# Performance work log

Hardware: AMD Instinct MI355X
Metric: run time of the kernel (lower is better)

The kernel has to match this reference:

```python
import jax, jax.numpy as jnp
import numpy as np

H, KV, DH = 16, 4, 64  # num_heads, num_kv_heads, head_dim


def setup_inputs() -> dict:
    key = jax.random.key(0)
    k1, k2, k3, k4, k5 = jax.random.split(key, 5)
    B, L, D = 1, 4096, 1024
    s = 0.02
    return {
        "x": jax.random.normal(k1, (B, L, D), dtype=jnp.float32),
        "Wq": jax.random.normal(k2, (D, H * DH), dtype=jnp.float32) * s,
        "Wk": jax.random.normal(k3, (D, KV * DH), dtype=jnp.float32) * s,
        "Wv": jax.random.normal(k4, (D, KV * DH), dtype=jnp.float32) * s,
        "Wo": jax.random.normal(k5, (H * DH, D), dtype=jnp.float32) * s,
    }


def _rotate_half(t):
    t1, t2 = t[..., : DH // 2], t[..., DH // 2 :]
    return jnp.concatenate([-t2, t1], axis=-1)


def reference(x, Wq, Wk, Wv, Wo):
    B, L, D = x.shape
    G = H // KV  # query heads per kv head
    q = (x @ Wq).reshape(B, L, H, DH)
    k = (x @ Wk).reshape(B, L, KV, DH)
    v = (x @ Wv).reshape(B, L, KV, DH)

    # RoPE: inv_freq over even dims, angles duplicated across both halves
    inv_freq = 1.0 / (10000.0 ** (jnp.arange(0, DH, 2, dtype=jnp.float32) / DH))
    t = jnp.arange(L, dtype=jnp.float32)
    freqs = t[:, None] * inv_freq[None, :]                 # [L, DH/2]
    emb = jnp.concatenate([freqs, freqs], axis=-1)[None, :, None, :]  # [1,L,1,DH]
    cos, sin = jnp.cos(emb), jnp.sin(emb)
    q = q * cos + _rotate_half(q) * sin
    k = k * cos + _rotate_half(k) * sin

    # GQA: query head h attends with kv head h // G (repeat_interleave layout)
    qg = q.reshape(B, L, KV, G, DH)
    scale = DH ** -0.5
    attn = jnp.einsum("bqkgd,bskd->bkgqs", qg, k) * scale  # [B,KV,G,L,L]
    attn = jax.nn.softmax(attn, axis=-1)
    out = jnp.einsum("bkgqs,bskd->bqkgd", attn, v).reshape(B, L, H * DH)
    return out @ Wo
```

## Files before the change

### kernel.cpp

```cpp
#include <hip/hip_runtime.h>
#include <math.h>

#define L 4096
#define D 1024
#define H 16
#define KV 4
#define DH 64

typedef __attribute__((ext_vector_type(8))) short bf16x8;
typedef __attribute__((ext_vector_type(4))) float f32x4;
typedef __attribute__((ext_vector_type(16))) float f32x16;
typedef __attribute__((ext_vector_type(2))) unsigned int u32x2;

static __device__ __forceinline__ unsigned short f2bf(float f) {
    unsigned u = __float_as_uint(f);
    u = (u + 0x7FFF + ((u >> 16) & 1)) >> 16;
    return (unsigned short)u;
}

static __device__ __forceinline__ bf16x8 mk8(unsigned a, unsigned b, unsigned c, unsigned d) {
    union { unsigned u[4]; bf16x8 v; } x;
    x.u[0] = a; x.u[1] = b; x.u[2] = c; x.u[3] = d;
    return x.v;
}

#define EXP2F(x) __builtin_amdgcn_exp2f(x)
#define ZERO16 ((f32x16){0.f,0.f,0.f,0.f,0.f,0.f,0.f,0.f,0.f,0.f,0.f,0.f,0.f,0.f,0.f,0.f})

#define GLD16(src, dst) \
    __builtin_amdgcn_global_load_lds((__attribute__((address_space(1))) void*)(src), \
                                     (__attribute__((address_space(3))) void*)(dst), 16, 0, 0)

__global__ __launch_bounds__(256) void prep_kernel(
        const float* __restrict__ x,  const float* __restrict__ Wq,
        const float* __restrict__ Wk, const float* __restrict__ Wv,
        const float* __restrict__ Wo,
        unsigned short* __restrict__ xb, unsigned short* __restrict__ WqkvT,
        unsigned short* __restrict__ WoT) {
    const int b = blockIdx.x, tid = threadIdx.x;
    if (b < 4096) {
        int i = (b * 256 + tid) * 4;
        float4 v = *(const float4*)&x[i];
        ushort4 o;
        o.x = f2bf(v.x); o.y = f2bf(v.y); o.z = f2bf(v.z); o.w = f2bf(v.w);
        *(ushort4*)&xb[i] = o;
        return;
    }
    __shared__ float t[32][33];
    const float* src; unsigned short* dst; int N, n0, k0;
    if (b < 5120)      { int tq = b - 4096; src = Wq; dst = WqkvT;                     N = 1024; n0 = (tq & 31) * 32; k0 = (tq >> 5) * 32; }
    else if (b < 5376) { int tq = b - 5120; src = Wk; dst = WqkvT + (size_t)1024*1024; N = 256;  n0 = (tq & 7)  * 32; k0 = (tq >> 3) * 32; }
    else if (b < 5632) { int tq = b - 5376; src = Wv; dst = WqkvT + (size_t)1280*1024; N = 256;  n0 = (tq & 7)  * 32; k0 = (tq >> 3) * 32; }
    else               { int tq = b - 5632; src = Wo; dst = WoT;                       N = 1024; n0 = (tq & 31) * 32; k0 = (tq >> 5) * 32; }
    const int tx = tid & 31, ty = tid >> 5;
    #pragma unroll
    for (int j = 0; j < 4; ++j)
        t[ty + 8 * j][tx] = src[(size_t)(k0 + ty + 8 * j) * N + n0 + tx];
    __syncthreads();
    #pragma unroll
    for (int j = 0; j < 4; ++j)
        dst[(size_t)(n0 + ty + 8 * j) * 1024 + k0 + tx] = f2bf(t[tx][ty + 8 * j]);
}

__global__ __launch_bounds__(256) void gemm_bf16(const unsigned short* __restrict__ A,
                                                 const unsigned short* __restrict__ BT,
                                                 float* __restrict__ C,
                                                 int M, int N, int K) {
    __shared__ unsigned short As[128 * 32];
    __shared__ unsigned short Bs[128 * 32];

    const int tid  = threadIdx.x;
    const int w    = tid >> 6;
    const int lane = tid & 63;
    const int c    = lane & 15;
    const int quad = lane >> 4;
    const int wy = w >> 1, wx = w & 1;
    const int row0 = blockIdx.y * 128;
    const int col0 = blockIdx.x * 128;

    const int ld_row = w * 16 + (lane >> 2);
    const int ld_col = (lane & 3) * 8;

    f32x4 acc[4][4];
    #pragma unroll
    for (int mt = 0; mt < 4; ++mt)
        #pragma unroll
        for (int nt = 0; nt < 4; ++nt)
            acc[mt][nt] = (f32x4){0.f, 0.f, 0.f, 0.f};

    for (int k0 = 0; k0 < K; k0 += 32) {
        __syncthreads();
        GLD16(&A [(size_t)(row0 + ld_row)      * K + k0 + ld_col], &As[w * 512]);
        GLD16(&A [(size_t)(row0 + ld_row + 64) * K + k0 + ld_col], &As[w * 512 + 2048]);
        GLD16(&BT[(size_t)(col0 + ld_row)      * K + k0 + ld_col], &Bs[w * 512]);
        GLD16(&BT[(size_t)(col0 + ld_row + 64) * K + k0 + ld_col], &Bs[w * 512 + 2048]);
        __syncthreads();

        bf16x8 af[4], bfr[4];
        #pragma unroll
        for (int mt = 0; mt < 4; ++mt)
            af[mt] = *(const bf16x8*)&As[(wy * 64 + mt * 16 + c) * 32 + quad * 8];
        #pragma unroll
        for (int nt = 0; nt < 4; ++nt)
            bfr[nt] = *(const bf16x8*)&Bs[(wx * 64 + nt * 16 + c) * 32 + quad * 8];

        #pragma unroll
        for (int mt = 0; mt < 4; ++mt)
            #pragma unroll
            for (int nt = 0; nt < 4; ++nt)
                acc[mt][nt] = __builtin_amdgcn_mfma_f32_16x16x32_bf16(af[mt], bfr[nt], acc[mt][nt], 0, 0, 0);
    }

    #pragma unroll
    for (int mt = 0; mt < 4; ++mt)
        #pragma unroll
        for (int nt = 0; nt < 4; ++nt)
            #pragma unroll
            for (int r = 0; r < 4; ++r)
                C[(size_t)(row0 + wy * 64 + mt * 16 + quad * 4 + r) * N
                  + col0 + wx * 64 + nt * 16 + c] = acc[mt][nt][r];
}

__global__ __launch_bounds__(256) void gemm_qkv_rope(
        const unsigned short* __restrict__ A,
        const unsigned short* __restrict__ BT,
        unsigned short* __restrict__ qb,
        unsigned short* __restrict__ kbuf,
        unsigned short* __restrict__ vbT) {
    __shared__ unsigned short As[128 * 32];
    __shared__ unsigned short Bs[128 * 32];

    const int tid  = threadIdx.x;
    const int w    = tid >> 6;
    const int lane = tid & 63;
    const int c    = lane & 15;
    const int quad = lane >> 4;
    const int wy = w >> 1, wx = w & 1;
    const int row0 = blockIdx.y * 128;
    const int col0 = blockIdx.x * 128;

    const int ld_row = w * 16 + (lane >> 2);
    const int ld_col = (lane & 3) * 8;

    f32x4 acc[4][4];
    #pragma unroll
    for (int mt = 0; mt < 4; ++mt)
        #pragma unroll
        for (int nt = 0; nt < 4; ++nt)
            acc[mt][nt] = (f32x4){0.f, 0.f, 0.f, 0.f};

    for (int k0 = 0; k0 < 1024; k0 += 32) {
        __syncthreads();
        GLD16(&A [(size_t)(row0 + ld_row)      * 1024 + k0 + ld_col], &As[w * 512]);
        GLD16(&A [(size_t)(row0 + ld_row + 64) * 1024 + k0 + ld_col], &As[w * 512 + 2048]);
        GLD16(&BT[(size_t)(col0 + ld_row)      * 1024 + k0 + ld_col], &Bs[w * 512]);
        GLD16(&BT[(size_t)(col0 + ld_row + 64) * 1024 + k0 + ld_col], &Bs[w * 512 + 2048]);
        __syncthreads();

        bf16x8 af[4], bfr[4];
        #pragma unroll
        for (int mt = 0; mt < 4; ++mt)
            af[mt] = *(const bf16x8*)&As[(wy * 64 + mt * 16 + c) * 32 + quad * 8];
        #pragma unroll
        for (int nt = 0; nt < 4; ++nt)
            bfr[nt] = *(const bf16x8*)&Bs[(wx * 64 + nt * 16 + c) * 32 + quad * 8];

        #pragma unroll
        for (int mt = 0; mt < 4; ++mt)
            #pragma unroll
            for (int nt = 0; nt < 4; ++nt)
                acc[mt][nt] = __builtin_amdgcn_mfma_f32_16x16x32_bf16(af[mt], bfr[nt], acc[mt][nt], 0, 0, 0);
    }

    const int colb = col0 + wx * 64;
    if (colb < 1280) {
        unsigned short* dst; int hh, hstride; float scale;
        if (colb < 1024) { dst = qb;   hh = colb >> 6;          hstride = H;  scale = 0.18033688011112042f; }
        else             { dst = kbuf; hh = (colb - 1024) >> 6; hstride = KV; scale = 1.0f; }
        #pragma unroll
        for (int nt = 0; nt < 2; ++nt) {
            int d = nt * 16 + c;
            float invf = EXP2F((float)d * -0.4152410118609203f);
            #pragma unroll
            for (int mt = 0; mt < 4; ++mt)
                #pragma unroll
                for (int r = 0; r < 4; ++r) {
                    int l = row0 + wy * 64 + mt * 16 + quad * 4 + r;
                    float ang = (float)l * invf;
                    float sn = __sinf(ang), cs = __cosf(ang);
                    float x1 = acc[mt][nt][r], x2 = acc[mt][nt + 2][r];
                    dst[((size_t)l * hstride + hh) * DH + d]      = f2bf((x1 * cs - x2 * sn) * scale);
                    dst[((size_t)l * hstride + hh) * DH + d + 32] = f2bf((x2 * cs + x1 * sn) * scale);
                }
        }
    } else {
        int vh = (colb - 1280) >> 6;
        #pragma unroll
        for (int nt = 0; nt < 4; ++nt)
            #pragma unroll
            for (int mt = 0; mt < 4; ++mt) {
                int l = row0 + wy * 64 + mt * 16 + quad * 4;
                ushort4 o;
                o.x = f2bf(acc[mt][nt][0]); o.y = f2bf(acc[mt][nt][1]);
                o.z = f2bf(acc[mt][nt][2]); o.w = f2bf(acc[mt][nt][3]);
                *(ushort4*)&vbT[(size_t)(vh * DH + nt * 16 + c) * L + l] = o;
            }
    }
}

__global__ __attribute__((amdgpu_flat_work_group_size(512, 512), amdgpu_waves_per_eu(2)))
void attn_mfma_kernel(
        const unsigned short* __restrict__ qb,
        const unsigned short* __restrict__ kb,
        const unsigned short* __restrict__ vbT,
        unsigned short* __restrict__ ob) {
    __shared__ __align__(16) float Ep[4][64][64];
    __shared__ __align__(16) float Rs[8][2][32];

    const int tid  = threadIdx.x;
    const int w    = tid >> 6;
    const int lane = tid & 63;
    const int c32  = lane & 31;
    const int hi   = lane >> 5;
    const int g    = w >> 2;
    const int kv = blockIdx.y;
    const int h  = kv * 4 + (w & 3);
    const int q0 = blockIdx.x * 64;
    const int s_base = g * 2048;

    bf16x8 qf[2][4];
    {
        const unsigned short* qbase = qb + ((size_t)(q0 + c32) * H + h) * DH + hi * 8;
        #pragma unroll
        for (int qt = 0; qt < 2; ++qt)
            #pragma unroll
            for (int kd = 0; kd < 4; ++kd)
                qf[qt][kd] = *(const bf16x8*)&qbase[qt * 32 * H * DH + kd * 16];
    }

    f32x16 oacc[2][2];
    #pragma unroll
    for (int qt = 0; qt < 2; ++qt)
        #pragma unroll
        for (int dt = 0; dt < 2; ++dt)
            oacc[qt][dt] = ZERO16;
    float rsum[2] = {0.f, 0.f};

    const unsigned short* kbase  = kb  + ((size_t)(s_base + c32) * KV + kv) * DH + hi * 8;
    const unsigned short* vTbase = vbT + (size_t)(kv * DH) * L + s_base + hi * 8;

    bf16x8 kf[2][4];
    #pragma unroll
    for (int a = 0; a < 2; ++a)
        #pragma unroll
        for (int kd = 0; kd < 4; ++kd)
            kf[a][kd] = *(const bf16x8*)&kbase[a * 32 * KV * DH + kd * 16];

    for (int it = 0; it < 32; ++it) {
        bf16x8 vfrag[2][4];
        #pragma unroll
        for (int dt = 0; dt < 2; ++dt)
            #pragma unroll
            for (int ck = 0; ck < 4; ++ck)
                vfrag[dt][ck] = *(const bf16x8*)&vTbase[(size_t)(dt * 32 + c32) * L
                                                        + it * 64 + ck * 16];

        const int itn = (it + 1) & 31;

        #pragma unroll
        for (int kt2 = 0; kt2 < 2; ++kt2) {
            bf16x8 pf[2][2];
            #pragma unroll
            for (int qt = 0; qt < 2; ++qt) {
                f32x16 s = ZERO16;
                #pragma unroll
                for (int kd = 0; kd < 4; ++kd)
                    s = __builtin_amdgcn_mfma_f32_32x32x16_bf16(kf[kt2][kd], qf[qt][kd], s, 0, 0, 0);
                float p[16];
                #pragma unroll
                for (int r = 0; r < 16; ++r)
                    p[r] = __uint_as_float(__float_as_uint(EXP2F(s[r])) & 0xFFFF0000u);
                float t0 = (p[0] + p[1]) + (p[2] + p[3]);
                float t1 = (p[4] + p[5]) + (p[6] + p[7]);
                float t2 = (p[8] + p[9]) + (p[10] + p[11]);
                float t3 = (p[12] + p[13]) + (p[14] + p[15]);
                rsum[qt] += (t0 + t1) + (t2 + t3);
                unsigned u[8];
                #pragma unroll
                for (int i = 0; i < 8; ++i)
                    u[i] = __builtin_amdgcn_perm(__float_as_uint(p[2 * i + 1]),
                                                 __float_as_uint(p[2 * i]), 0x07060302u);
                #pragma unroll
                for (int f = 0; f < 2; ++f) {
                    u32x2 e0 = __builtin_amdgcn_permlane32_swap(u[4 * f + 0], u[4 * f + 2], false, false);
                    u32x2 e1 = __builtin_amdgcn_permlane32_swap(u[4 * f + 1], u[4 * f + 3], false, false);
                    pf[qt][f] = mk8(e0.x, e1.x, e0.y, e1.y);
                }
            }
            if (kt2 == 1) {
                #pragma unroll
                for (int a = 0; a < 2; ++a)
                    #pragma unroll
                    for (int kd = 0; kd < 4; ++kd)
                        kf[a][kd] = *(const bf16x8*)&kbase[((size_t)itn * 64 + a * 32) * KV * DH + kd * 16];
            }
            __builtin_amdgcn_s_setprio(1);
            #pragma unroll
            for (int dt = 0; dt < 2; ++dt)
                #pragma unroll
                for (int f = 0; f < 2; ++f) {
                    bf16x8 vf = vfrag[dt][kt2 * 2 + f];
                    #pragma unroll
                    for (int qt = 0; qt < 2; ++qt)
                        oacc[qt][dt] = __builtin_amdgcn_mfma_f32_32x32x16_bf16(pf[qt][f], vf, oacc[qt][dt], 0, 0, 0);
                }
            __builtin_amdgcn_s_setprio(0);
        }
    }

    #pragma unroll
    for (int qt = 0; qt < 2; ++qt) {
        u32x2 e = __builtin_amdgcn_permlane32_swap(__float_as_uint(rsum[qt]),
                                                   __float_as_uint(rsum[qt]), false, false);
        float tot = __uint_as_float(e.x) + __uint_as_float(e.y);
        Rs[w][qt][c32] = tot;
    }
    if (g == 1) {
        #pragma unroll
        for (int qt = 0; qt < 2; ++qt)
            #pragma unroll
            for (int dt = 0; dt < 2; ++dt) {
                const int d = dt * 32 + c32;
                #pragma unroll
                for (int rr = 0; rr < 4; ++rr) {
                    const int gq = (qt * 8 + 2 * rr + hi) ^ (d & 15);
                    f32x4 val = {oacc[qt][dt][rr * 4 + 0], oacc[qt][dt][rr * 4 + 1],
                                 oacc[qt][dt][rr * 4 + 2], oacc[qt][dt][rr * 4 + 3]};
                    *(f32x4*)&Ep[w - 4][d][gq * 4] = val;
                }
            }
    }
    __syncthreads();
    if (g == 0) {
        #pragma unroll
        for (int qt = 0; qt < 2; ++qt)
            #pragma unroll
            for (int dt = 0; dt < 2; ++dt) {
                const int d = dt * 32 + c32;
                #pragma unroll
                for (int rr = 0; rr < 4; ++rr) {
                    const int gq = (qt * 8 + 2 * rr + hi) ^ (d & 15);
                    f32x4 val = *(const f32x4*)&Ep[w][d][gq * 4];
                    oacc[qt][dt][rr * 4 + 0] += val[0];
                    oacc[qt][dt][rr * 4 + 1] += val[1];
                    oacc[qt][dt][rr * 4 + 2] += val[2];
                    oacc[qt][dt][rr * 4 + 3] += val[3];
                }
            }
        #pragma unroll
        for (int qt = 0; qt < 2; ++qt)
            #pragma unroll
            for (int rr = 0; rr < 4; ++rr) {
                f32x4 ra = *(const f32x4*)&Rs[w][qt][8 * rr + 4 * hi];
                f32x4 rb = *(const f32x4*)&Rs[w + 4][qt][8 * rr + 4 * hi];
                #pragma unroll
                for (int i = 0; i < 4; ++i) {
                    float inv = 1.0f / (ra[i] + rb[i]);
                    int row = q0 + qt * 32 + 8 * rr + 4 * hi + i;
                    #pragma unroll
                    for (int dt = 0; dt < 2; ++dt)
                        ob[(size_t)row * (H * DH) + h * DH + dt * 32 + c32] =
                            f2bf(oacc[qt][dt][rr * 4 + i] * inv);
                }
            }
    }
}

extern "C" void kernel_launch(void* const* d_in, const int* in_sizes, int n_in,
                              void* d_out, int out_size, void* d_ws, size_t ws_size,
                              hipStream_t stream) {
    const float* x  = (const float*)d_in[0];
    const float* Wq = (const float*)d_in[1];
    const float* Wk = (const float*)d_in[2];
    const float* Wv = (const float*)d_in[3];
    const float* Wo = (const float*)d_in[4];
    float* out = (float*)d_out;

    char* ws = (char*)d_ws;
    unsigned short* xb    = (unsigned short*)ws;
    unsigned short* ob    = xb;
    unsigned short* qb    = (unsigned short*)(ws + 8388608);
    unsigned short* kb    = (unsigned short*)(ws + 16777216);
    unsigned short* vbT   = (unsigned short*)(ws + 18874368);
    unsigned short* WqkvT = (unsigned short*)(ws + 20971520);
    unsigned short* WoT   = (unsigned short*)(ws + 24117248);

    dim3 blk(256);

    prep_kernel<<<6656, blk, 0, stream>>>(x, Wq, Wk, Wv, Wo, xb, WqkvT, WoT);

    gemm_qkv_rope<<<dim3(12, 32), blk, 0, stream>>>(xb, WqkvT, qb, kb, vbT);

    attn_mfma_kernel<<<dim3(L / 64, KV), dim3(512), 0, stream>>>(qb, kb, vbT, ob);

    gemm_bf16<<<dim3(D / 128, L / 128), blk, 0, stream>>>(ob, WoT, out, L, D, D);
}
```

Measured before the change: 256.1 us.

## Halve attention query tile, stage V via LDS double buffer, raise occupancy

The attention kernel now handles 32 queries per block instead of 64, which halves the accumulator and Q registers and doubles the grid. V tiles are loaded asynchronously into a double-buffered, XOR-swizzled LDS buffer shared by the four heads of a KV group, instead of each wave loading them from global memory. The waves-per-EU hint goes from 2 to 4. Together these aim for higher occupancy and less redundant V traffic, at the cost of a barrier per iteration and K reloads amortised over fewer queries.

```diff
diff --git a/kernel.cpp b/kernel.cpp
--- a/kernel.cpp
+++ b/kernel.cpp
@@ -208,14 +208,14 @@
     }
 }
 
-__global__ __attribute__((amdgpu_flat_work_group_size(512, 512), amdgpu_waves_per_eu(2)))
+__global__ __attribute__((amdgpu_flat_work_group_size(512, 512), amdgpu_waves_per_eu(4)))
 void attn_mfma_kernel(
         const unsigned short* __restrict__ qb,
         const unsigned short* __restrict__ kb,
         const unsigned short* __restrict__ vbT,
         unsigned short* __restrict__ ob) {
-    __shared__ __align__(16) float Ep[4][64][64];
-    __shared__ __align__(16) float Rs[8][2][32];
+    __shared__ __align__(16) unsigned short Vt[2][2][64][64];
+    __shared__ __align__(16) float Rs[8][32];
 
     const int tid  = threadIdx.x;
     const int w    = tid >> 6;
@@ -225,29 +225,29 @@
     const int g    = w >> 2;
     const int kv = blockIdx.y;
     const int h  = kv * 4 + (w & 3);
-    const int q0 = blockIdx.x * 64;
+    const int q0 = blockIdx.x * 32;
     const int s_base = g * 2048;
 
-    bf16x8 qf[2][4];
+    const int vrow0 = (w & 3) * 16;
+    const int d0 = vrow0 + (lane >> 3);
+    const unsigned short* vsrc0 = vbT + (size_t)(kv * DH + d0) * L + s_base
+                                  + (((lane & 7) ^ (d0 & 7)) << 3);
+    const unsigned short* vsrc1 = vbT + (size_t)(kv * DH + d0 + 8) * L + s_base
+                                  + (((lane & 7) ^ ((d0 + 8) & 7)) << 3);
+
+    bf16x8 qf[4];
     {
         const unsigned short* qbase = qb + ((size_t)(q0 + c32) * H + h) * DH + hi * 8;
         #pragma unroll
-        for (int qt = 0; qt < 2; ++qt)
-            #pragma unroll
-            for (int kd = 0; kd < 4; ++kd)
-                qf[qt][kd] = *(const bf16x8*)&qbase[qt * 32 * H * DH + kd * 16];
-    }
-
-    f32x16 oacc[2][2];
-    #pragma unroll
-    for (int qt = 0; qt < 2; ++qt)
-        #pragma unroll
-        for (int dt = 0; dt < 2; ++dt)
-            oacc[qt][dt] = ZERO16;
-    float rsum[2] = {0.f, 0.f};
-
-    const unsigned short* kbase  = kb  + ((size_t)(s_base + c32) * KV + kv) * DH + hi * 8;
-    const unsigned short* vTbase = vbT + (size_t)(kv * DH) * L + s_base + hi * 8;
+        for (int kd = 0; kd < 4; ++kd)
+            qf[kd] = *(const bf16x8*)&qbase[kd * 16];
+    }
+
+    f32x16 oacc[2];
+    oacc[0] = ZERO16; oacc[1] = ZERO16;
+    float rsum = 0.f;
+
+    const unsigned short* kbase = kb + ((size_t)(s_base + c32) * KV + kv) * DH + hi * 8;
 
     bf16x8 kf[2][4];
     #pragma unroll
@@ -255,47 +255,47 @@
         #pragma unroll
         for (int kd = 0; kd < 4; ++kd)
             kf[a][kd] = *(const bf16x8*)&kbase[a * 32 * KV * DH + kd * 16];
+    GLD16(vsrc0, &Vt[g][0][vrow0][0]);
+    GLD16(vsrc1, &Vt[g][0][vrow0 + 8][0]);
 
     for (int it = 0; it < 32; ++it) {
-        bf16x8 vfrag[2][4];
-        #pragma unroll
-        for (int dt = 0; dt < 2; ++dt)
-            #pragma unroll
-            for (int ck = 0; ck < 4; ++ck)
-                vfrag[dt][ck] = *(const bf16x8*)&vTbase[(size_t)(dt * 32 + c32) * L
-                                                        + it * 64 + ck * 16];
-
+        const int buf = it & 1;
+        __syncthreads();
+
+        if (it != 31) {
+            GLD16(vsrc0 + (it + 1) * 64, &Vt[g][buf ^ 1][vrow0][0]);
+            GLD16(vsrc1 + (it + 1) * 64, &Vt[g][buf ^ 1][vrow0 + 8][0]);
+        }
         const int itn = (it + 1) & 31;
 
         #pragma unroll
         for (int kt2 = 0; kt2 < 2; ++kt2) {
-            bf16x8 pf[2][2];
-            #pragma unroll
-            for (int qt = 0; qt < 2; ++qt) {
-                f32x16 s = ZERO16;
-                #pragma unroll
-                for (int kd = 0; kd < 4; ++kd)
-                    s = __builtin_amdgcn_mfma_f32_32x32x16_bf16(kf[kt2][kd], qf[qt][kd], s, 0, 0, 0);
-                float p[16];
-                #pragma unroll
-                for (int r = 0; r < 16; ++r)
-                    p[r] = __uint_as_float(__float_as_uint(EXP2F(s[r])) & 0xFFFF0000u);
-                float t0 = (p[0] + p[1]) + (p[2] + p[3]);
-                float t1 = (p[4] + p[5]) + (p[6] + p[7]);
-                float t2 = (p[8] + p[9]) + (p[10] + p[11]);
-                float t3 = (p[12] + p[13]) + (p[14] + p[15]);
-                rsum[qt] += (t0 + t1) + (t2 + t3);
-                unsigned u[8];
-                #pragma unroll
-                for (int i = 0; i < 8; ++i)
-                    u[i] = __builtin_amdgcn_perm(__float_as_uint(p[2 * i + 1]),
-                                                 __float_as_uint(p[2 * i]), 0x07060302u);
-                #pragma unroll
-                for (int f = 0; f < 2; ++f) {
-                    u32x2 e0 = __builtin_amdgcn_permlane32_swap(u[4 * f + 0], u[4 * f + 2], false, false);
-                    u32x2 e1 = __builtin_amdgcn_permlane32_swap(u[4 * f + 1], u[4 * f + 3], false, false);
-                    pf[qt][f] = mk8(e0.x, e1.x, e0.y, e1.y);
-                }
+            f32x16 s = ZERO16;
+            #pragma unroll
+            for (int kd = 0; kd < 4; ++kd)
+                s = __builtin_amdgcn_mfma_f32_32x32x16_bf16(kf[kt2][kd], qf[kd], s, 0, 0, 0);
+
+            unsigned u[8];
+            #pragma unroll
+            for (int hf = 0; hf < 2; ++hf) {
+                float ph[8];
+                #pragma unroll
+                for (int r = 0; r < 8; ++r)
+                    ph[r] = __uint_as_float(__float_as_uint(EXP2F(s[hf * 8 + r])) & 0xFFFF0000u);
+                float t0 = (ph[0] + ph[1]) + (ph[2] + ph[3]);
+                float t1 = (ph[4] + ph[5]) + (ph[6] + ph[7]);
+                rsum += t0 + t1;
+                #pragma unroll
+                for (int i = 0; i < 4; ++i)
+                    u[hf * 4 + i] = __builtin_amdgcn_perm(__float_as_uint(ph[2 * i + 1]),
+                                                          __float_as_uint(ph[2 * i]), 0x07060302u);
+            }
+            bf16x8 pf[2];
+            #pragma unroll
+            for (int f = 0; f < 2; ++f) {
+                u32x2 e0 = __builtin_amdgcn_permlane32_swap(u[4 * f + 0], u[4 * f + 2], false, false);
+                u32x2 e1 = __builtin_amdgcn_permlane32_swap(u[4 * f + 1], u[4 * f + 3], false, false);
+                pf[f] = mk8(e0.x, e1.x, e0.y, e1.y);
             }
             if (kt2 == 1) {
                 #pragma unroll
@@ -309,70 +309,65 @@
             for (int dt = 0; dt < 2; ++dt)
                 #pragma unroll
                 for (int f = 0; f < 2; ++f) {
-                    bf16x8 vf = vfrag[dt][kt2 * 2 + f];
-                    #pragma unroll
-                    for (int qt = 0; qt < 2; ++qt)
-                        oacc[qt][dt] = __builtin_amdgcn_mfma_f32_32x32x16_bf16(pf[qt][f], vf, oacc[qt][dt], 0, 0, 0);
+                    bf16x8 vf = *(const bf16x8*)&Vt[g][buf][dt * 32 + c32]
+                                    [(((kt2 * 4 + f * 2 + hi) ^ (c32 & 7)) << 3)];
+                    oacc[dt] = __builtin_amdgcn_mfma_f32_32x32x16_bf16(pf[f], vf, oacc[dt], 0, 0, 0);
                 }
             __builtin_amdgcn_s_setprio(0);
         }
     }
 
-    #pragma unroll
-    for (int qt = 0; qt < 2; ++qt) {
-        u32x2 e = __builtin_amdgcn_permlane32_swap(__float_as_uint(rsum[qt]),
-                                                   __float_as_uint(rsum[qt]), false, false);
-        float tot = __uint_as_float(e.x) + __uint_as_float(e.y);
-        Rs[w][qt][c32] = tot;
-    }
+    float tot;
+    {
+        u32x2 e = __builtin_amdgcn_permlane32_swap(__float_as_uint(rsum),
+                                                   __float_as_uint(rsum), false, false);
+        tot = __uint_as_float(e.x) + __uint_as_float(e.y);
+    }
+    __syncthreads();
+    float (*Ep)[64][32] = (float (*)[64][32])(&Vt[0][0][0][0]);
+    Rs[w][c32] = tot;
     if (g == 1) {
         #pragma unroll
-        for (int qt = 0; qt < 2; ++qt)
-            #pragma unroll
-            for (int dt = 0; dt < 2; ++dt) {
-                const int d = dt * 32 + c32;
-                #pragma unroll
-                for (int rr = 0; rr < 4; ++rr) {
-                    const int gq = (qt * 8 + 2 * rr + hi) ^ (d & 15);
-                    f32x4 val = {oacc[qt][dt][rr * 4 + 0], oacc[qt][dt][rr * 4 + 1],
-                                 oacc[qt][dt][rr * 4 + 2], oacc[qt][dt][rr * 4 + 3]};
-                    *(f32x4*)&Ep[w - 4][d][gq * 4] = val;
-                }
-            }
+        for (int dt = 0; dt < 2; ++dt) {
+            const int d = dt * 32 + c32;
+            #pragma unroll
+            for (int rr = 0; rr < 4; ++rr) {
+                const int gq = (2 * rr + hi) ^ (d & 7);
+                f32x4 val = {oacc[dt][rr * 4 + 0], oacc[dt][rr * 4 + 1],
+                             oacc[dt][rr * 4 + 2], oacc[dt][rr * 4 + 3]};
+                *(f32x4*)&Ep[w - 4][d][gq * 4] = val;
+            }
+        }
     }
     __syncthreads();
     if (g == 0) {
         #pragma unroll
-        for (int qt = 0; qt < 2; ++qt)
-            #pragma unroll
-            for (int dt = 0; dt < 2; ++dt) {
-                const int d = dt * 32 + c32;
-                #pragma unroll
-                for (int rr = 0; rr < 4; ++rr) {
-                    const int gq = (qt * 8 + 2 * rr + hi) ^ (d & 15);
-                    f32x4 val = *(const f32x4*)&Ep[w][d][gq * 4];
-                    oacc[qt][dt][rr * 4 + 0] += val[0];
-                    oacc[qt][dt][rr * 4 + 1] += val[1];
-                    oacc[qt][dt][rr * 4 + 2] += val[2];
-                    oacc[qt][dt][rr * 4 + 3] += val[3];
-                }
-            }
-        #pragma unroll
-        for (int qt = 0; qt < 2; ++qt)
+        for (int dt = 0; dt < 2; ++dt) {
+            const int d = dt * 32 + c32;
             #pragma unroll
             for (int rr = 0; rr < 4; ++rr) {
-                f32x4 ra = *(const f32x4*)&Rs[w][qt][8 * rr + 4 * hi];
-                f32x4 rb = *(const f32x4*)&Rs[w + 4][qt][8 * rr + 4 * hi];
-                #pragma unroll
-                for (int i = 0; i < 4; ++i) {
-                    float inv = 1.0f / (ra[i] + rb[i]);
-                    int row = q0 + qt * 32 + 8 * rr + 4 * hi + i;
-                    #pragma unroll
-                    for (int dt = 0; dt < 2; ++dt)
-                        ob[(size_t)row * (H * DH) + h * DH + dt * 32 + c32] =
-                            f2bf(oacc[qt][dt][rr * 4 + i] * inv);
-                }
-            }
+                const int gq = (2 * rr + hi) ^ (d & 7);
+                f32x4 val = *(const f32x4*)&Ep[w][d][gq * 4];
+                oacc[dt][rr * 4 + 0] += val[0];
+                oacc[dt][rr * 4 + 1] += val[1];
+                oacc[dt][rr * 4 + 2] += val[2];
+                oacc[dt][rr * 4 + 3] += val[3];
+            }
+        }
+        #pragma unroll
+        for (int rr = 0; rr < 4; ++rr) {
+            f32x4 ra = *(const f32x4*)&Rs[w][8 * rr + 4 * hi];
+            f32x4 rb = *(const f32x4*)&Rs[w + 4][8 * rr + 4 * hi];
+            #pragma unroll
+            for (int i = 0; i < 4; ++i) {
+                float inv = 1.0f / (ra[i] + rb[i]);
+                int row = q0 + 8 * rr + 4 * hi + i;
+                #pragma unroll
+                for (int dt = 0; dt < 2; ++dt)
+                    ob[(size_t)row * (H * DH) + h * DH + dt * 32 + c32] =
+                        f2bf(oacc[dt][rr * 4 + i] * inv);
+            }
+        }
     }
 }
 
@@ -401,7 +396,7 @@
 
     gemm_qkv_rope<<<dim3(12, 32), blk, 0, stream>>>(xb, WqkvT, qb, kb, vbT);
 
-    attn_mfma_kernel<<<dim3(L / 64, KV), dim3(512), 0, stream>>>(qb, kb, vbT, ob);
+    attn_mfma_kernel<<<dim3(L / 32, KV), dim3(512), 0, stream>>>(qb, kb, vbT, ob);
 
     gemm_bf16<<<dim3(D / 128, L / 128), blk, 0, stream>>>(ob, WoT, out, L, D, D);
 }
```

Result: slower. 279.1 us (+9.0%).

## Stage V tiles in double-buffered swizzled LDS shared across head waves

Applied to the files above, without the earlier changes.

Each group of four waves (one per query head sharing a KV head) previously loaded identical V fragments from global memory on its own. Now V tiles of 128 keys are loaded once per group with direct global-to-LDS loads (GLD16) into a double-buffered, XOR-swizzled LDS buffer. Waves then read their fragments from LDS. The K register tile is doubled to 128 keys per iteration, and the epilogue LDS buffer is aliased onto the V staging area. This cuts redundant global/L2 traffic but adds a block-wide barrier every iteration and more register pressure from the larger K tile.

```diff
diff --git a/kernel.cpp b/kernel.cpp
--- a/kernel.cpp
+++ b/kernel.cpp
@@ -214,7 +214,7 @@
         const unsigned short* __restrict__ kb,
         const unsigned short* __restrict__ vbT,
         unsigned short* __restrict__ ob) {
-    __shared__ __align__(16) float Ep[4][64][64];
+    __shared__ __align__(16) unsigned short Vt[2][2][64][128];
     __shared__ __align__(16) float Rs[8][2][32];
 
     const int tid  = threadIdx.x;
@@ -228,6 +228,16 @@
     const int q0 = blockIdx.x * 64;
     const int s_base = g * 2048;
 
+    const int vrow0 = (w & 3) * 16;
+    const unsigned short* vsrc[4];
+    #pragma unroll
+    for (int s = 0; s < 4; ++s) {
+        int d = vrow0 + s * 4 + (lane >> 4);
+        int swz = (d & 15) ^ (((d >> 4) & 1) << 2);
+        vsrc[s] = vbT + (size_t)(kv * DH + d) * L + s_base + (((lane & 15) ^ swz) << 3);
+    }
+    const int swzr = (c32 & 15) ^ ((c32 >> 4) << 2);
+
     bf16x8 qf[2][4];
     {
         const unsigned short* qbase = qb + ((size_t)(q0 + c32) * H + h) * DH + hi * 8;
@@ -246,29 +256,31 @@
             oacc[qt][dt] = ZERO16;
     float rsum[2] = {0.f, 0.f};
 
-    const unsigned short* kbase  = kb  + ((size_t)(s_base + c32) * KV + kv) * DH + hi * 8;
-    const unsigned short* vTbase = vbT + (size_t)(kv * DH) * L + s_base + hi * 8;
-
-    bf16x8 kf[2][4];
-    #pragma unroll
-    for (int a = 0; a < 2; ++a)
+    const unsigned short* kbase = kb + ((size_t)(s_base + c32) * KV + kv) * DH + hi * 8;
+
+    bf16x8 kf[4][4];
+    #pragma unroll
+    for (int a = 0; a < 4; ++a)
         #pragma unroll
         for (int kd = 0; kd < 4; ++kd)
             kf[a][kd] = *(const bf16x8*)&kbase[a * 32 * KV * DH + kd * 16];
-
-    for (int it = 0; it < 32; ++it) {
-        bf16x8 vfrag[2][4];
-        #pragma unroll
-        for (int dt = 0; dt < 2; ++dt)
-            #pragma unroll
-            for (int ck = 0; ck < 4; ++ck)
-                vfrag[dt][ck] = *(const bf16x8*)&vTbase[(size_t)(dt * 32 + c32) * L
-                                                        + it * 64 + ck * 16];
-
-        const int itn = (it + 1) & 31;
-
-        #pragma unroll
-        for (int kt2 = 0; kt2 < 2; ++kt2) {
+    #pragma unroll
+    for (int s = 0; s < 4; ++s)
+        GLD16(vsrc[s], &Vt[g][0][vrow0 + s * 4][0]);
+
+    for (int it = 0; it < 16; ++it) {
+        const int buf = it & 1;
+        __syncthreads();
+
+        if (it != 15) {
+            #pragma unroll
+            for (int s = 0; s < 4; ++s)
+                GLD16(vsrc[s] + (size_t)(it + 1) * 128, &Vt[g][buf ^ 1][vrow0 + s * 4][0]);
+        }
+        const int itn = (it + 1) & 15;
+
+        #pragma unroll
+        for (int kt2 = 0; kt2 < 4; ++kt2) {
             bf16x8 pf[2][2];
             #pragma unroll
             for (int qt = 0; qt < 2; ++qt) {
@@ -297,19 +309,20 @@
                     pf[qt][f] = mk8(e0.x, e1.x, e0.y, e1.y);
                 }
             }
-            if (kt2 == 1) {
-                #pragma unroll
-                for (int a = 0; a < 2; ++a)
+            if (kt2 == 3) {
+                #pragma unroll
+                for (int a = 0; a < 4; ++a)
                     #pragma unroll
                     for (int kd = 0; kd < 4; ++kd)
-                        kf[a][kd] = *(const bf16x8*)&kbase[((size_t)itn * 64 + a * 32) * KV * DH + kd * 16];
+                        kf[a][kd] = *(const bf16x8*)&kbase[((size_t)itn * 128 + a * 32) * KV * DH + kd * 16];
             }
             __builtin_amdgcn_s_setprio(1);
             #pragma unroll
             for (int dt = 0; dt < 2; ++dt)
                 #pragma unroll
                 for (int f = 0; f < 2; ++f) {
-                    bf16x8 vf = vfrag[dt][kt2 * 2 + f];
+                    bf16x8 vf = *(const bf16x8*)&Vt[g][buf][dt * 32 + c32]
+                                    [((kt2 * 4 + f * 2 + hi) ^ swzr) << 3];
                     #pragma unroll
                     for (int qt = 0; qt < 2; ++qt)
                         oacc[qt][dt] = __builtin_amdgcn_mfma_f32_32x32x16_bf16(pf[qt][f], vf, oacc[qt][dt], 0, 0, 0);
@@ -325,6 +338,8 @@
         float tot = __uint_as_float(e.x) + __uint_as_float(e.y);
         Rs[w][qt][c32] = tot;
     }
+    __syncthreads();
+    float (*Ep)[64][64] = (float (*)[64][64])&Vt[0][0][0][0];
     if (g == 1) {
         #pragma unroll
         for (int qt = 0; qt < 2; ++qt)
```

New measurement: 381.1 us. 1.49x slower.

## Split attention key range four ways and stage V tiles through LDS

Applied to the files above, without the earlier changes.

The attention block grows from 512 to 1024 threads, so the key dimension is split across four wave groups of 1024 keys each instead of two groups of 2048. V is now loaded into swizzled, double-buffered LDS tiles with async global-to-LDS copies (GLD16) rather than per-lane strided global reads. The end-of-kernel reduction combines four partial accumulators and row sums through LDS. The aim is more waves per CU for latency hiding and coalesced V traffic, at the cost of a barrier every iteration and a longer, multi-barrier reduction.

```diff
diff --git a/kernel.cpp b/kernel.cpp
--- a/kernel.cpp
+++ b/kernel.cpp
@@ -208,14 +208,14 @@
     }
 }
 
-__global__ __attribute__((amdgpu_flat_work_group_size(512, 512), amdgpu_waves_per_eu(2)))
+__global__ __attribute__((amdgpu_flat_work_group_size(1024, 1024), amdgpu_waves_per_eu(4)))
 void attn_mfma_kernel(
         const unsigned short* __restrict__ qb,
         const unsigned short* __restrict__ kb,
         const unsigned short* __restrict__ vbT,
         unsigned short* __restrict__ ob) {
-    __shared__ __align__(16) float Ep[4][64][64];
-    __shared__ __align__(16) float Rs[8][2][32];
+    __shared__ __align__(16) unsigned short Vt[4][2][64][64];
+    __shared__ __align__(16) float Rs[16][2][32];
 
     const int tid  = threadIdx.x;
     const int w    = tid >> 6;
@@ -226,7 +226,14 @@
     const int kv = blockIdx.y;
     const int h  = kv * 4 + (w & 3);
     const int q0 = blockIdx.x * 64;
-    const int s_base = g * 2048;
+    const int s_base = g * 1024;
+
+    const int vrow0 = (w & 3) * 16;
+    const int d0 = vrow0 + (lane >> 3);
+    const unsigned short* vsrc0 = vbT + (size_t)(kv * DH + d0) * L + s_base
+                                  + (((lane & 7) ^ (d0 & 7)) << 3);
+    const unsigned short* vsrc1 = vbT + (size_t)(kv * DH + d0 + 8) * L + s_base
+                                  + (((lane & 7) ^ ((d0 + 8) & 7)) << 3);
 
     bf16x8 qf[2][4];
     {
@@ -246,8 +253,7 @@
             oacc[qt][dt] = ZERO16;
     float rsum[2] = {0.f, 0.f};
 
-    const unsigned short* kbase  = kb  + ((size_t)(s_base + c32) * KV + kv) * DH + hi * 8;
-    const unsigned short* vTbase = vbT + (size_t)(kv * DH) * L + s_base + hi * 8;
+    const unsigned short* kbase = kb + ((size_t)(s_base + c32) * KV + kv) * DH + hi * 8;
 
     bf16x8 kf[2][4];
     #pragma unroll
@@ -255,17 +261,18 @@
         #pragma unroll
         for (int kd = 0; kd < 4; ++kd)
             kf[a][kd] = *(const bf16x8*)&kbase[a * 32 * KV * DH + kd * 16];
-
-    for (int it = 0; it < 32; ++it) {
-        bf16x8 vfrag[2][4];
-        #pragma unroll
-        for (int dt = 0; dt < 2; ++dt)
-            #pragma unroll
-            for (int ck = 0; ck < 4; ++ck)
-                vfrag[dt][ck] = *(const bf16x8*)&vTbase[(size_t)(dt * 32 + c32) * L
-                                                        + it * 64 + ck * 16];
-
-        const int itn = (it + 1) & 31;
+    GLD16(vsrc0, &Vt[g][0][vrow0][0]);
+    GLD16(vsrc1, &Vt[g][0][vrow0 + 8][0]);
+
+    for (int it = 0; it < 16; ++it) {
+        const int buf = it & 1;
+        __syncthreads();
+
+        if (it != 15) {
+            GLD16(vsrc0 + (it + 1) * 64, &Vt[g][buf ^ 1][vrow0][0]);
+            GLD16(vsrc1 + (it + 1) * 64, &Vt[g][buf ^ 1][vrow0 + 8][0]);
+        }
+        const int itn = (it + 1) & 15;
 
         #pragma unroll
         for (int kt2 = 0; kt2 < 2; ++kt2) {
@@ -309,7 +316,8 @@
             for (int dt = 0; dt < 2; ++dt)
                 #pragma unroll
                 for (int f = 0; f < 2; ++f) {
-                    bf16x8 vf = vfrag[dt][kt2 * 2 + f];
+                    bf16x8 vf = *(const bf16x8*)&Vt[g][buf][dt * 32 + c32]
+                                    [(((kt2 * 4 + f * 2 + hi) ^ (c32 & 7)) << 3)];
                     #pragma unroll
                     for (int qt = 0; qt < 2; ++qt)
                         oacc[qt][dt] = __builtin_amdgcn_mfma_f32_32x32x16_bf16(pf[qt][f], vf, oacc[qt][dt], 0, 0, 0);
@@ -325,47 +333,50 @@
         float tot = __uint_as_float(e.x) + __uint_as_float(e.y);
         Rs[w][qt][c32] = tot;
     }
-    if (g == 1) {
+    __syncthreads();
+    float* Ep = (float*)&Vt[0][0][0][0];
+    #pragma unroll
+    for (int qt = 0; qt < 2; ++qt)
+        #pragma unroll
+        for (int dt = 0; dt < 2; ++dt) {
+            if (g > 0) {
+                float* dst = Ep + (size_t)(w - 4) * 1024 + lane * 16;
+                #pragma unroll
+                for (int k = 0; k < 4; ++k) {
+                    f32x4 val = {oacc[qt][dt][k * 4 + 0], oacc[qt][dt][k * 4 + 1],
+                                 oacc[qt][dt][k * 4 + 2], oacc[qt][dt][k * 4 + 3]};
+                    *(f32x4*)&dst[k * 4] = val;
+                }
+            }
+            __syncthreads();
+            if (g == 0) {
+                #pragma unroll
+                for (int part = 1; part <= 3; ++part) {
+                    const float* src = Ep + (size_t)(part * 4 + w - 4) * 1024 + lane * 16;
+                    #pragma unroll
+                    for (int k = 0; k < 4; ++k) {
+                        f32x4 val = *(const f32x4*)&src[k * 4];
+                        oacc[qt][dt][k * 4 + 0] += val[0];
+                        oacc[qt][dt][k * 4 + 1] += val[1];
+                        oacc[qt][dt][k * 4 + 2] += val[2];
+                        oacc[qt][dt][k * 4 + 3] += val[3];
+                    }
+                }
+            }
+            __syncthreads();
+        }
+    if (g == 0) {
         #pragma unroll
         for (int qt = 0; qt < 2; ++qt)
             #pragma unroll
-            for (int dt = 0; dt < 2; ++dt) {
-                const int d = dt * 32 + c32;
-                #pragma unroll
-                for (int rr = 0; rr < 4; ++rr) {
-                    const int gq = (qt * 8 + 2 * rr + hi) ^ (d & 15);
-                    f32x4 val = {oacc[qt][dt][rr * 4 + 0], oacc[qt][dt][rr * 4 + 1],
-                                 oacc[qt][dt][rr * 4 + 2], oacc[qt][dt][rr * 4 + 3]};
-                    *(f32x4*)&Ep[w - 4][d][gq * 4] = val;
-                }
-            }
-    }
-    __syncthreads();
-    if (g == 0) {
-        #pragma unroll
-        for (int qt = 0; qt < 2; ++qt)
-            #pragma unroll
-            for (int dt = 0; dt < 2; ++dt) {
-                const int d = dt * 32 + c32;
-                #pragma unroll
-                for (int rr = 0; rr < 4; ++rr) {
-                    const int gq = (qt * 8 + 2 * rr + hi) ^ (d & 15);
-                    f32x4 val = *(const f32x4*)&Ep[w][d][gq * 4];
-                    oacc[qt][dt][rr * 4 + 0] += val[0];
-                    oacc[qt][dt][rr * 4 + 1] += val[1];
-                    oacc[qt][dt][rr * 4 + 2] += val[2];
-                    oacc[qt][dt][rr * 4 + 3] += val[3];
-                }
-            }
-        #pragma unroll
-        for (int qt = 0; qt < 2; ++qt)
-            #pragma unroll
             for (int rr = 0; rr < 4; ++rr) {
-                f32x4 ra = *(const f32x4*)&Rs[w][qt][8 * rr + 4 * hi];
-                f32x4 rb = *(const f32x4*)&Rs[w + 4][qt][8 * rr + 4 * hi];
+                f32x4 r0 = *(const f32x4*)&Rs[w     ][qt][8 * rr + 4 * hi];
+                f32x4 r1 = *(const f32x4*)&Rs[w +  4][qt][8 * rr + 4 * hi];
+                f32x4 r2 = *(const f32x4*)&Rs[w +  8][qt][8 * rr + 4 * hi];
+                f32x4 r3 = *(const f32x4*)&Rs[w + 12][qt][8 * rr + 4 * hi];
                 #pragma unroll
                 for (int i = 0; i < 4; ++i) {
-                    float inv = 1.0f / (ra[i] + rb[i]);
+                    float inv = 1.0f / (r0[i] + r1[i] + r2[i] + r3[i]);
                     int row = q0 + qt * 32 + 8 * rr + 4 * hi + i;
                     #pragma unroll
                     for (int dt = 0; dt < 2; ++dt)
@@ -401,7 +412,7 @@
 
     gemm_qkv_rope<<<dim3(12, 32), blk, 0, stream>>>(xb, WqkvT, qb, kb, vbT);
 
-    attn_mfma_kernel<<<dim3(L / 64, KV), dim3(512), 0, stream>>>(qb, kb, vbT, ob);
+    attn_mfma_kernel<<<dim3(L / 64, KV), dim3(1024), 0, stream>>>(qb, kb, vbT, ob);
 
     gemm_bf16<<<dim3(D / 128, L / 128), blk, 0, stream>>>(ob, WoT, out, L, D, D);
 }
```

After: 1.001 ms. +291.0%, slower.
